# Kernel optimization log

Hardware: AMD Instinct MI355X
Metric: run time of the kernel (lower is better)

The kernel has to match this reference:

```python
import jax, jax.numpy as jnp
import numpy as np
import math

N_HEAD = 8
HIDDEN = 512
HEAD_DIM = HIDDEN // N_HEAD


def _grid_neighborhood_mask(num_nodes: int) -> jnp.ndarray:
    """Encoder mask: 2D grid adjacency (4-neighborhood) + self, with one
    extra global token (row/col 0) that attends to / is attended by all."""
    n = int(math.sqrt(num_nodes - 1))
    idx = np.arange(n * n)
    r, c = idx // n, idx % n
    # manhattan distance <= 1 <=> grid edge or self
    d = np.abs(r[:, None] - r[None, :]) + np.abs(c[:, None] - c[None, :])
    m = d <= 1  # [n*n, n*n] bool
    m = np.pad(m, ((1, 0), (1, 0)), constant_values=True)  # global token
    return jnp.asarray(m)


def setup_inputs() -> dict:
    key = jax.random.key(0)
    k_x, k_q, k_k, k_v, k_o = jax.random.split(key, 5)
    B, N = 2, 64 * 64 + 1  # 4097 nodes (64x64 grid + global token)
    scale = 1.0 / math.sqrt(HIDDEN)
    x = jax.random.normal(k_x, (B, N, HIDDEN), dtype=jnp.float32)
    Wq = jax.random.normal(k_q, (HIDDEN, HIDDEN), dtype=jnp.float32) * scale
    Wk = jax.random.normal(k_k, (HIDDEN, HIDDEN), dtype=jnp.float32) * scale
    Wv = jax.random.normal(k_v, (HIDDEN, HIDDEN), dtype=jnp.float32) * scale
    Wo = jax.random.normal(k_o, (HIDDEN, HIDDEN), dtype=jnp.float32) * scale
    return {"x": x, "Wq": Wq, "Wk": Wk, "Wv": Wv, "Wo": Wo}


def reference(x, Wq, Wk, Wv, Wo):
    B, N, D = x.shape
    mask = _grid_neighborhood_mask(N)  # [N, N] bool, static shape

    def split_heads(y):  # [B,N,D] -> [B,H,N,Dh]
        return y.reshape(B, N, N_HEAD, HEAD_DIM).transpose(0, 2, 1, 3)

    # torch Linear (no bias): y = x @ W^T
    q = split_heads(jnp.einsum('bnd,ed->bne', x, Wq))
    k = split_heads(jnp.einsum('bnd,ed->bne', x, Wk))
    v = split_heads(jnp.einsum('bnd,ed->bne', x, Wv))

    scores = jnp.einsum('bhnd,bhmd->bhnm', q, k) / math.sqrt(HEAD_DIM)
    scores = jnp.where(mask, scores, -jnp.inf)
    probs = jax.nn.softmax(scores, axis=-1)  # every row has self=True
    attn = jnp.einsum('bhnm,bhmd->bhnd', probs, v)  # [B,H,N,Dh]

    attn = attn.transpose(0, 2, 1, 3).reshape(B, N, D)
    out = jnp.einsum('bnd,ed->bne', attn, Wo)  # dropout is identity (p=0/eval)
    return out
```

## Files before the change

### kernel.cpp

```cpp
#include <hip/hip_runtime.h>

#define DI __device__ __forceinline__

typedef __bf16 bf16x8 __attribute__((ext_vector_type(8)));
typedef float  f32x4  __attribute__((ext_vector_type(4)));
typedef unsigned short u16;
typedef unsigned int   u32;

constexpr int BATCH  = 2;
constexpr int NNODE  = 4097;
constexpr int M_REAL = BATCH * NNODE;
constexpr int M_PAD  = 8448;
constexpr int KDIM   = 512;

constexpr int JC     = 256;
constexpr int NCHUNK = (NNODE + JC - 1) / JC;
constexpr int NDB    = BATCH * 8 * NCHUNK;

DI float bf2f(u16 u)  { return __uint_as_float(((u32)u) << 16); }
DI float bflo(u32 v)  { return __uint_as_float(v << 16); }
DI float bfhi(u32 v)  { return __uint_as_float(v & 0xffff0000u); }
DI u16   f2bf(float f) {
  u32 u = __float_as_uint(f);
  u32 r = (u + 0x7fffu + ((u >> 16) & 1u)) >> 16;
  return (u16)r;
}

DI void gload_lds16(const void* g, void* l) {
  __builtin_amdgcn_global_load_lds(
      (const __attribute__((address_space(1))) u32*)g,
      (__attribute__((address_space(3))) u32*)l, 16, 0, 0);
}

constexpr int NCH_X  = M_PAD * KDIM / 8;
constexpr int NCH_WQ = 1536 * KDIM / 8;
constexpr int NCH_WO = 512 * KDIM / 8;

__global__ __launch_bounds__(256) void prep(
    const float* __restrict__ x,  const float* __restrict__ wq,
    const float* __restrict__ wk, const float* __restrict__ wv,
    const float* __restrict__ wo,
    u16* __restrict__ Xp, u16* __restrict__ Wqkv, u16* __restrict__ Wob) {
  int idx = blockIdx.x * 256 + threadIdx.x;
  const float* src = nullptr;
  u16* dst = nullptr;
  bool zero = false;
  if (idx < NCH_X) {
    int row = idx >> 6;
    dst = Xp + (size_t)idx * 8;
    if (row < M_REAL) src = x + (size_t)idx * 8; else zero = true;
  } else if (idx < NCH_X + NCH_WQ) {
    int t = idx - NCH_X;
    int row = t >> 6;
    dst = Wqkv + (size_t)t * 8;
    const float* W = row < 512 ? wq : (row < 1024 ? wk : wv);
    src = W + ((size_t)(row & 511) << 9) + ((t & 63) * 8);
  } else if (idx < NCH_X + NCH_WQ + NCH_WO) {
    int t = idx - NCH_X - NCH_WQ;
    dst = Wob + (size_t)t * 8;
    src = wo + (size_t)t * 8;
  } else {
    return;
  }
  u32 o[4];
  if (zero) {
    o[0] = o[1] = o[2] = o[3] = 0u;
  } else {
    float4 f0 = ((const float4*)src)[0];
    float4 f1 = ((const float4*)src)[1];
    o[0] = (u32)f2bf(f0.x) | ((u32)f2bf(f0.y) << 16);
    o[1] = (u32)f2bf(f0.z) | ((u32)f2bf(f0.w) << 16);
    o[2] = (u32)f2bf(f1.x) | ((u32)f2bf(f1.y) << 16);
    o[3] = (u32)f2bf(f1.z) | ((u32)f2bf(f1.w) << 16);
  }
  uint4 v; v.x = o[0]; v.y = o[1]; v.z = o[2]; v.w = o[3];
  *(uint4*)dst = v;
}

__global__ __launch_bounds__(512, 2) void gemm256(
    const u16* __restrict__ A, const u16* __restrict__ B,
    u16* __restrict__ C) {
  __shared__ __align__(16) u16 SM[65536];
  const int tid  = threadIdx.x;
  const int lane = tid & 63;
  const int wid  = tid >> 6;
  const int wm   = wid >> 2;
  const int wn   = wid & 3;
  const int m0 = blockIdx.x * 256;
  const int n0 = blockIdx.y * 256;

  const int l15 = lane & 15, l7 = lane & 7, lg = lane >> 4;

  const int srow = tid >> 3;
  const int scol = ((tid & 7) ^ (srow & 7)) << 3;
  const u16* Ag = A + (size_t)(m0 + srow) * KDIM + scol;
  const u16* Bg = B + (size_t)(n0 + srow) * KDIM + scol;

  const int kx0 = ((lg * 8)        ^ (l7 << 3));
  const int kx1 = (((4 | lg) * 8)  ^ (l7 << 3));
  const int aBase = wm * 8192 + l15 * 64;
  const int bBase = 32768 + (wn >> 1) * 8192 + ((wn & 1) * 64 + l15) * 64;

  f32x4 acc[8][4] = {};

  constexpr int NT = KDIM / 64;

  auto stage = [&](int t, int buf) {
    const int ab = buf * 32768;
    const u16* ga = Ag + t * 64;
    const u16* gb = Bg + t * 64;
#pragma unroll
    for (int h = 0; h < 4; ++h) {
      gload_lds16(ga + (size_t)h * 64 * KDIM, (char*)SM + ab + h * 8192 + tid * 16);
      gload_lds16(gb + (size_t)h * 64 * KDIM, (char*)SM + 65536 + ab + h * 8192 + tid * 16);
    }
  };

  stage(0, 0);

  for (int t = 0; t < NT; ++t) {
    const int buf = t & 1;
    if (t + 1 < NT) {
      stage(t + 1, buf ^ 1);
      asm volatile("s_waitcnt vmcnt(8)" ::: "memory");
    } else {
      asm volatile("s_waitcnt vmcnt(0)" ::: "memory");
    }
    asm volatile("s_barrier" ::: "memory");

    const int aB = aBase + buf * 16384;
    const int bB = bBase + buf * 16384;

    bf16x8 bfr[4][2];
#pragma unroll
    for (int ni = 0; ni < 4; ++ni) {
      bfr[ni][0] = *(const bf16x8*)&SM[bB + ni * 1024 + kx0];
      bfr[ni][1] = *(const bf16x8*)&SM[bB + ni * 1024 + kx1];
    }
#pragma unroll
    for (int qm = 0; qm < 2; ++qm) {
      bf16x8 af[4][2];
#pragma unroll
      for (int i = 0; i < 4; ++i) {
        const int mi = qm * 4 + i;
        af[i][0] = *(const bf16x8*)&SM[aB + mi * 1024 + kx0];
        af[i][1] = *(const bf16x8*)&SM[aB + mi * 1024 + kx1];
      }
      __builtin_amdgcn_s_setprio(1);
#pragma unroll
      for (int i = 0; i < 4; ++i)
#pragma unroll
        for (int ni = 0; ni < 4; ++ni) {
          acc[qm*4+i][ni] = __builtin_amdgcn_mfma_f32_16x16x32_bf16(
              af[i][0], bfr[ni][0], acc[qm*4+i][ni], 0, 0, 0);
          acc[qm*4+i][ni] = __builtin_amdgcn_mfma_f32_16x16x32_bf16(
              af[i][1], bfr[ni][1], acc[qm*4+i][ni], 0, 0, 0);
        }
      __builtin_amdgcn_s_setprio(0);
    }
    asm volatile("s_barrier" ::: "memory");
  }

  const int cr = lg * 4, cc = l15;
#pragma unroll
  for (int mi = 0; mi < 8; ++mi)
#pragma unroll
    for (int j = 0; j < 4; ++j) {
      const int row = m0 + wm * 128 + mi * 16 + cr + j;
#pragma unroll
      for (int ni = 0; ni < 4; ++ni) {
        const int col = n0 + wn * 64 + ni * 16 + cc;
        C[(size_t)row * 1536 + col] = f2bf(acc[mi][ni][j]);
      }
    }
}

template <int N, bool OUT_F32>
__global__ __launch_bounds__(256) void gemm_bt(
    const u16* __restrict__ A, const u16* __restrict__ B,
    u16* __restrict__ Cb, float* __restrict__ Cf) {
  __shared__ __align__(16) u16 As[128 * 64];
  __shared__ __align__(16) u16 Bs[128 * 64];
  const int tid  = threadIdx.x;
  const int lane = tid & 63;
  const int wm = ((tid >> 6) >> 1) * 64;
  const int wn = ((tid >> 6) & 1) * 64;
  const int m0 = blockIdx.x * 128;
  const int n0 = blockIdx.y * 128;

  f32x4 acc[4][4] = {};

  const int rstg = tid >> 3;
  const int cstg = (tid & 7) * 8;
  const u16* Ag = A + (size_t)(m0 + rstg) * KDIM + cstg;
  const u16* Bg = B + (size_t)(n0 + rstg) * KDIM + cstg;
  char* AsB = (char*)As + tid * 16;
  char* BsB = (char*)Bs + tid * 16;

  for (int kt = 0; kt < KDIM; kt += 64) {
#pragma unroll
    for (int inst = 0; inst < 4; ++inst) {
      gload_lds16(Ag + (size_t)inst * 32 * KDIM + kt, AsB + inst * 4096);
      gload_lds16(Bg + (size_t)inst * 32 * KDIM + kt, BsB + inst * 4096);
    }
    __syncthreads();
#pragma unroll
    for (int kc = 0; kc < 2; ++kc) {
      const int ko = kc * 32 + (lane >> 4) * 8;
      bf16x8 af[4], bfr[4];
#pragma unroll
      for (int mi = 0; mi < 4; ++mi)
        af[mi] = *(const bf16x8*)&As[(wm + mi * 16 + (lane & 15)) * 64 + ko];
#pragma unroll
      for (int ni = 0; ni < 4; ++ni)
        bfr[ni] = *(const bf16x8*)&Bs[(wn + ni * 16 + (lane & 15)) * 64 + ko];
#pragma unroll
      for (int mi = 0; mi < 4; ++mi)
#pragma unroll
        for (int ni = 0; ni < 4; ++ni)
          acc[mi][ni] = __builtin_amdgcn_mfma_f32_16x16x32_bf16(
              af[mi], bfr[ni], acc[mi][ni], 0, 0, 0);
    }
    __syncthreads();
  }

  const int cr = (lane >> 4) * 4;
  const int cc = lane & 15;
#pragma unroll
  for (int mi = 0; mi < 4; ++mi) {
#pragma unroll
    for (int j = 0; j < 4; ++j) {
      const int row = m0 + wm + mi * 16 + cr + j;
      if (OUT_F32 && row >= M_REAL) continue;
#pragma unroll
      for (int ni = 0; ni < 4; ++ni) {
        const int col = n0 + wn + ni * 16 + cc;
        if constexpr (OUT_F32)
          Cf[(size_t)row * N + col] = acc[mi][ni][j];
        else
          Cb[(size_t)row * N + col] = f2bf(acc[mi][ni][j]);
      }
    }
  }
}

__global__ __launch_bounds__(256) void attn(const u16* __restrict__ QKV,
                                            u16* __restrict__ O,
                                            float* __restrict__ Part) {
  const int tid = threadIdx.x;
  if (blockIdx.x < NDB) {
    __shared__ float qs[64];
    __shared__ float ev[JC];
    __shared__ float red[256];
    const int db = blockIdx.x;
    const int b  = db / (8 * NCHUNK);
    const int rm = db % (8 * NCHUNK);
    const int h  = rm / NCHUNK;
    const int ch = rm % NCHUNK;
    const int j0 = ch * JC;
    const size_t base = (size_t)b * NNODE;

    if (tid < 64) qs[tid] = bf2f(QKV[base * 1536 + h * 64 + tid]);
    __syncthreads();

    const int j = j0 + tid;
    float s = -3e38f;
    if (j < NNODE) {
      const uint4* kp4 = (const uint4*)(QKV + (base + j) * 1536 + 512 + h * 64);
      float a = 0.f;
#pragma unroll
      for (int q8 = 0; q8 < 8; ++q8) {
        uint4 kv = kp4[q8];
        int d = q8 * 8;
        a += qs[d+0]*bflo(kv.x) + qs[d+1]*bfhi(kv.x)
           + qs[d+2]*bflo(kv.y) + qs[d+3]*bfhi(kv.y)
           + qs[d+4]*bflo(kv.z) + qs[d+5]*bfhi(kv.z)
           + qs[d+6]*bflo(kv.w) + qs[d+7]*bfhi(kv.w);
      }
      s = a * 0.125f;
    }
    red[tid] = s;
    __syncthreads();
    for (int st = 128; st > 0; st >>= 1) {
      if (tid < st) red[tid] = fmaxf(red[tid], red[tid + st]);
      __syncthreads();
    }
    const float mx = red[0];
    __syncthreads();
    const float e = (j < NNODE) ? __expf(s - mx) : 0.f;
    ev[tid] = e;
    red[tid] = e;
    __syncthreads();
    for (int st = 128; st > 0; st >>= 1) {
      if (tid < st) red[tid] += red[tid + st];
      __syncthreads();
    }
    const float ssum = red[0];
    __syncthreads();

    const int w = tid >> 6, lane = tid & 63;
    const int js = lane >> 3, dg = lane & 7;
    float oa[8] = {};
#pragma unroll
    for (int jj = 0; jj < 8; ++jj) {
      const int li = w * 64 + jj * 8 + js;
      const int jv = j0 + li;
      if (jv < NNODE) {
        const float we = ev[li];
        const uint4 vv = *(const uint4*)(QKV + (base + jv) * 1536 + 1024 + h * 64 + dg * 8);
        oa[0] += we * bflo(vv.x); oa[1] += we * bfhi(vv.x);
        oa[2] += we * bflo(vv.y); oa[3] += we * bfhi(vv.y);
        oa[4] += we * bflo(vv.z); oa[5] += we * bfhi(vv.z);
        oa[6] += we * bflo(vv.w); oa[7] += we * bfhi(vv.w);
      }
    }
#pragma unroll
    for (int m = 8; m <= 32; m <<= 1)
#pragma unroll
      for (int t = 0; t < 8; ++t) oa[t] += __shfl_xor(oa[t], m);
    __syncthreads();
    if (lane < 8) {
#pragma unroll
      for (int t = 0; t < 8; ++t) red[w * 64 + lane * 8 + t] = oa[t];
    }
    __syncthreads();
    float* P = Part + ((size_t)((b * 8 + h) * NCHUNK + ch)) * 66;
    if (tid == 0) { P[0] = mx; P[1] = ssum; }
    if (tid < 64)
      P[2 + tid] = red[tid] + red[64 + tid] + red[128 + tid] + red[192 + tid];
    return;
  }

  const int obid = blockIdx.x - NDB;
  const int sb   = ((obid & 7) << 8) | (obid >> 3);
  const int wid  = sb * 4 + (tid >> 6);
  const int lane = tid & 63;
  const int b = wid >> 12;
  const int g = wid & 4095;
  const int i = g + 1;
  const int r = g >> 6, c = g & 63;
  const size_t base = (size_t)b * NNODE;

  int  jn[6];
  bool vd[6];
  jn[0] = 0;                     vd[0] = true;
  jn[1] = i;                     vd[1] = true;
  jn[2] = (c > 0)  ? i - 1  : i; vd[2] = (c > 0);
  jn[3] = (c < 63) ? i + 1  : i; vd[3] = (c < 63);
  jn[4] = (r > 0)  ? i - 64 : i; vd[4] = (r > 0);
  jn[5] = (r < 63) ? i + 64 : i; vd[5] = (r < 63);

  const uint4 qv = *(const uint4*)(QKV + (base + i) * 1536 + lane * 8);
  float qf[8] = { bflo(qv.x), bfhi(qv.x), bflo(qv.y), bfhi(qv.y),
                  bflo(qv.z), bfhi(qv.z), bflo(qv.w), bfhi(qv.w) };

  float sc[6];
#pragma unroll
  for (int n = 0; n < 6; ++n) {
    const uint4 kv = *(const uint4*)(QKV + (base + jn[n]) * 1536 + 512 + lane * 8);
    float p = qf[0]*bflo(kv.x) + qf[1]*bfhi(kv.x)
            + qf[2]*bflo(kv.y) + qf[3]*bfhi(kv.y)
            + qf[4]*bflo(kv.z) + qf[5]*bfhi(kv.z)
            + qf[6]*bflo(kv.w) + qf[7]*bfhi(kv.w);
    p += __shfl_xor(p, 1);
    p += __shfl_xor(p, 2);
    p += __shfl_xor(p, 4);
    sc[n] = p * 0.125f;
  }
  float mx = -1e30f;
#pragma unroll
  for (int n = 0; n < 6; ++n) if (vd[n]) mx = fmaxf(mx, sc[n]);
  float pw[6], den = 0.f;
#pragma unroll
  for (int n = 0; n < 6; ++n) {
    pw[n] = vd[n] ? __expf(sc[n] - mx) : 0.f;
    den += pw[n];
  }
  const float inv = 1.f / den;

  float oa[8] = {};
#pragma unroll
  for (int n = 0; n < 6; ++n) {
    const uint4 vv = *(const uint4*)(QKV + (base + jn[n]) * 1536 + 1024 + lane * 8);
    const float w = pw[n];
    oa[0] += w * bflo(vv.x); oa[1] += w * bfhi(vv.x);
    oa[2] += w * bflo(vv.y); oa[3] += w * bfhi(vv.y);
    oa[4] += w * bflo(vv.z); oa[5] += w * bfhi(vv.z);
    oa[6] += w * bflo(vv.w); oa[7] += w * bfhi(vv.w);
  }
  uint4 ov;
  ov.x = (u32)f2bf(oa[0] * inv) | ((u32)f2bf(oa[1] * inv) << 16);
  ov.y = (u32)f2bf(oa[2] * inv) | ((u32)f2bf(oa[3] * inv) << 16);
  ov.z = (u32)f2bf(oa[4] * inv) | ((u32)f2bf(oa[5] * inv) << 16);
  ov.w = (u32)f2bf(oa[6] * inv) | ((u32)f2bf(oa[7] * inv) << 16);
  *(uint4*)(O + (base + i) * 512 + lane * 8) = ov;
}

__global__ __launch_bounds__(64) void attn_fin(const float* __restrict__ Part,
                                               u16* __restrict__ O) {
  const int b = blockIdx.x >> 3, h = blockIdx.x & 7;
  const int d = threadIdx.x;
  const float* P = Part + ((size_t)(b * 8 + h) * NCHUNK) * 66;
  float m = -3e38f;
  for (int c = 0; c < NCHUNK; ++c) m = fmaxf(m, P[c * 66]);
  float s = 0.f, o = 0.f;
  for (int c = 0; c < NCHUNK; ++c) {
    const float ex = __expf(P[c * 66] - m);
    s += P[c * 66 + 1] * ex;
    o += P[c * 66 + 2 + d] * ex;
  }
  O[(size_t)b * NNODE * 512 + h * 64 + d] = f2bf(o / s);
}

extern "C" void kernel_launch(void* const* d_in, const int* in_sizes, int n_in,
                              void* d_out, int out_size, void* d_ws, size_t ws_size,
                              hipStream_t stream) {
  (void)in_sizes; (void)n_in; (void)out_size; (void)ws_size;
  const float* x  = (const float*)d_in[0];
  const float* wq = (const float*)d_in[1];
  const float* wk = (const float*)d_in[2];
  const float* wv = (const float*)d_in[3];
  const float* wo = (const float*)d_in[4];
  float* out = (float*)d_out;

  char* ws = (char*)d_ws;
  u16* Xp   = (u16*)ws;  ws += (size_t)M_PAD * 512 * 2;
  u16* Wqkv = (u16*)ws;  ws += (size_t)1536 * 512 * 2;
  u16* Wob  = (u16*)ws;  ws += (size_t)512 * 512 * 2;
  u16* QKV  = (u16*)ws;  ws += (size_t)M_PAD * 1536 * 2;
  u16* ATT  = (u16*)ws;
  float* Part = (float*)Xp;

  prep<<<(NCH_X + NCH_WQ + NCH_WO) / 256, 256, 0, stream>>>(
      x, wq, wk, wv, wo, Xp, Wqkv, Wob);

  dim3 g1(M_PAD / 256, 1536 / 256);
  gemm256<<<g1, 512, 0, stream>>>(Xp, Wqkv, QKV);

  attn<<<NDB + 2048, 256, 0, stream>>>(QKV, ATT, Part);
  attn_fin<<<16, 64, 0, stream>>>(Part, ATT);

  dim3 g2(M_PAD / 128, 512 / 128);
  gemm_bt<512, true><<<g2, 256, 0, stream>>>(ATT, Wob, nullptr, out);
}
```

Measured before the change: 65.10 us.

## Fuse attention finalize via last-block atomic and double-buffer output GEMM

Removes the separate attn_fin launch: each global-token partial block bumps an atomic counter (zeroed in prep), and the last one merges all chunk partials. The output projection GEMM is rewritten with a double-buffered, XOR-swizzled LDS pipeline, raised priority around the MFMAs, two blocks per CU, and a grid cut to 65 row tiles, so padding rows beyond the real ones are skipped. Together these aim to save one kernel launch, hide global-to-LDS latency and reduce LDS bank conflicts. The cost is a serialized tail in the last attention block and the correctness burden of the atomic ordering and swizzle.

Measured after the change: 82.99 us. 1.27x slower.

```diff
diff --git a/kernel.cpp b/kernel.cpp
--- a/kernel.cpp
+++ b/kernel.cpp
@@ -40,8 +40,10 @@
     const float* __restrict__ x,  const float* __restrict__ wq,
     const float* __restrict__ wk, const float* __restrict__ wv,
     const float* __restrict__ wo,
-    u16* __restrict__ Xp, u16* __restrict__ Wqkv, u16* __restrict__ Wob) {
+    u16* __restrict__ Xp, u16* __restrict__ Wqkv, u16* __restrict__ Wob,
+    u32* __restrict__ Cnt) {
   int idx = blockIdx.x * 256 + threadIdx.x;
+  if (idx == 0) *Cnt = 0;
   const float* src = nullptr;
   u16* dst = nullptr;
   bool zero = false;
@@ -176,82 +178,110 @@
 }
 
 template <int N, bool OUT_F32>
-__global__ __launch_bounds__(256) void gemm_bt(
+__global__ __launch_bounds__(256, 2) void gemm128(
     const u16* __restrict__ A, const u16* __restrict__ B,
     u16* __restrict__ Cb, float* __restrict__ Cf) {
-  __shared__ __align__(16) u16 As[128 * 64];
-  __shared__ __align__(16) u16 Bs[128 * 64];
+  __shared__ __align__(16) u16 SM[32768];
   const int tid  = threadIdx.x;
   const int lane = tid & 63;
-  const int wm = ((tid >> 6) >> 1) * 64;
-  const int wn = ((tid >> 6) & 1) * 64;
-  const int m0 = blockIdx.x * 128;
-  const int n0 = blockIdx.y * 128;
+  const int wid  = tid >> 6;
+  const int wm   = wid >> 1, wn = wid & 1;
+  const int m0 = blockIdx.x * 128, n0 = blockIdx.y * 128;
+  const int l15 = lane & 15, l7 = lane & 7, lg = lane >> 4;
+
+  const int srow = tid >> 3;
+  const int scol = ((tid & 7) ^ (srow & 7)) << 3;
+  const u16* Ag = A + (size_t)(m0 + srow) * KDIM + scol;
+  const u16* Bg = B + (size_t)(n0 + srow) * KDIM + scol;
+
+  const int kx0 = ((lg * 8)       ^ (l7 << 3));
+  const int kx1 = (((4 | lg) * 8) ^ (l7 << 3));
+  const int aBase = wm * 4096 + l15 * 64;
+  const int bBase = 16384 + wn * 4096 + l15 * 64;
 
   f32x4 acc[4][4] = {};
-
-  const int rstg = tid >> 3;
-  const int cstg = (tid & 7) * 8;
-  const u16* Ag = A + (size_t)(m0 + rstg) * KDIM + cstg;
-  const u16* Bg = B + (size_t)(n0 + rstg) * KDIM + cstg;
-  char* AsB = (char*)As + tid * 16;
-  char* BsB = (char*)Bs + tid * 16;
-
-  for (int kt = 0; kt < KDIM; kt += 64) {
-#pragma unroll
-    for (int inst = 0; inst < 4; ++inst) {
-      gload_lds16(Ag + (size_t)inst * 32 * KDIM + kt, AsB + inst * 4096);
-      gload_lds16(Bg + (size_t)inst * 32 * KDIM + kt, BsB + inst * 4096);
-    }
-    __syncthreads();
-#pragma unroll
-    for (int kc = 0; kc < 2; ++kc) {
-      const int ko = kc * 32 + (lane >> 4) * 8;
-      bf16x8 af[4], bfr[4];
-#pragma unroll
-      for (int mi = 0; mi < 4; ++mi)
-        af[mi] = *(const bf16x8*)&As[(wm + mi * 16 + (lane & 15)) * 64 + ko];
-#pragma unroll
-      for (int ni = 0; ni < 4; ++ni)
-        bfr[ni] = *(const bf16x8*)&Bs[(wn + ni * 16 + (lane & 15)) * 64 + ko];
-#pragma unroll
-      for (int mi = 0; mi < 4; ++mi)
-#pragma unroll
-        for (int ni = 0; ni < 4; ++ni)
-          acc[mi][ni] = __builtin_amdgcn_mfma_f32_16x16x32_bf16(
-              af[mi], bfr[ni], acc[mi][ni], 0, 0, 0);
-    }
-    __syncthreads();
-  }
-
-  const int cr = (lane >> 4) * 4;
-  const int cc = lane & 15;
-#pragma unroll
-  for (int mi = 0; mi < 4; ++mi) {
+  constexpr int NT = KDIM / 64;
+
+  auto stage = [&](int t, int buf) {
+    const int ab = buf * 16384;
+    const u16* ga = Ag + t * 64;
+    const u16* gb = Bg + t * 64;
+#pragma unroll
+    for (int h = 0; h < 4; ++h) {
+      gload_lds16(ga + (size_t)h * 32 * KDIM, (char*)SM + ab + h * 4096 + tid * 16);
+      gload_lds16(gb + (size_t)h * 32 * KDIM, (char*)SM + 32768 + ab + h * 4096 + tid * 16);
+    }
+  };
+
+  stage(0, 0);
+
+  for (int t = 0; t < NT; ++t) {
+    const int buf = t & 1;
+    if (t + 1 < NT) {
+      stage(t + 1, buf ^ 1);
+      asm volatile("s_waitcnt vmcnt(8)" ::: "memory");
+    } else {
+      asm volatile("s_waitcnt vmcnt(0)" ::: "memory");
+    }
+    asm volatile("s_barrier" ::: "memory");
+
+    const int aB = aBase + buf * 8192;
+    const int bB = bBase + buf * 8192;
+
+    bf16x8 bfr[4][2];
+#pragma unroll
+    for (int ni = 0; ni < 4; ++ni) {
+      bfr[ni][0] = *(const bf16x8*)&SM[bB + ni * 1024 + kx0];
+      bfr[ni][1] = *(const bf16x8*)&SM[bB + ni * 1024 + kx1];
+    }
+    bf16x8 af[4][2];
+#pragma unroll
+    for (int i = 0; i < 4; ++i) {
+      af[i][0] = *(const bf16x8*)&SM[aB + i * 1024 + kx0];
+      af[i][1] = *(const bf16x8*)&SM[aB + i * 1024 + kx1];
+    }
+    __builtin_amdgcn_s_setprio(1);
+#pragma unroll
+    for (int i = 0; i < 4; ++i)
+#pragma unroll
+      for (int ni = 0; ni < 4; ++ni) {
+        acc[i][ni] = __builtin_amdgcn_mfma_f32_16x16x32_bf16(
+            af[i][0], bfr[ni][0], acc[i][ni], 0, 0, 0);
+        acc[i][ni] = __builtin_amdgcn_mfma_f32_16x16x32_bf16(
+            af[i][1], bfr[ni][1], acc[i][ni], 0, 0, 0);
+      }
+    __builtin_amdgcn_s_setprio(0);
+    asm volatile("s_barrier" ::: "memory");
+  }
+
+  const int cr = lg * 4, cc = l15;
+#pragma unroll
+  for (int mi = 0; mi < 4; ++mi)
 #pragma unroll
     for (int j = 0; j < 4; ++j) {
-      const int row = m0 + wm + mi * 16 + cr + j;
+      const int row = m0 + wm * 64 + mi * 16 + cr + j;
       if (OUT_F32 && row >= M_REAL) continue;
 #pragma unroll
       for (int ni = 0; ni < 4; ++ni) {
-        const int col = n0 + wn + ni * 16 + cc;
+        const int col = n0 + wn * 64 + ni * 16 + cc;
         if constexpr (OUT_F32)
           Cf[(size_t)row * N + col] = acc[mi][ni][j];
         else
           Cb[(size_t)row * N + col] = f2bf(acc[mi][ni][j]);
       }
     }
-  }
 }
 
 __global__ __launch_bounds__(256) void attn(const u16* __restrict__ QKV,
                                             u16* __restrict__ O,
-                                            float* __restrict__ Part) {
+                                            float* __restrict__ Part,
+                                            u32* __restrict__ Cnt) {
   const int tid = threadIdx.x;
   if (blockIdx.x < NDB) {
     __shared__ float qs[64];
     __shared__ float ev[JC];
     __shared__ float red[256];
+    __shared__ int lastFlag;
     const int db = blockIdx.x;
     const int b  = db / (8 * NCHUNK);
     const int rm = db % (8 * NCHUNK);
@@ -328,6 +358,27 @@
     if (tid == 0) { P[0] = mx; P[1] = ssum; }
     if (tid < 64)
       P[2 + tid] = red[tid] + red[64 + tid] + red[128 + tid] + red[192 + tid];
+
+    __threadfence();
+    if (tid == 0) lastFlag = (atomicAdd(Cnt, 1u) == (u32)(NDB - 1)) ? 1 : 0;
+    __syncthreads();
+    if (lastFlag) {
+      __threadfence();
+      const int d = tid & 63;
+      for (int task = tid >> 6; task < 16; task += 4) {
+        const int bb = task >> 3;
+        const float* P2 = Part + (size_t)task * NCHUNK * 66;
+        float m = -3e38f;
+        for (int c2 = 0; c2 < NCHUNK; ++c2) m = fmaxf(m, P2[c2 * 66]);
+        float ssm = 0.f, o = 0.f;
+        for (int c2 = 0; c2 < NCHUNK; ++c2) {
+          const float ex = __expf(P2[c2 * 66] - m);
+          ssm += P2[c2 * 66 + 1] * ex;
+          o   += P2[c2 * 66 + 2 + d] * ex;
+        }
+        O[(size_t)bb * NNODE * 512 + (task & 7) * 64 + d] = f2bf(o / ssm);
+      }
+    }
     return;
   }
 
@@ -396,22 +447,6 @@
   *(uint4*)(O + (base + i) * 512 + lane * 8) = ov;
 }
 
-__global__ __launch_bounds__(64) void attn_fin(const float* __restrict__ Part,
-                                               u16* __restrict__ O) {
-  const int b = blockIdx.x >> 3, h = blockIdx.x & 7;
-  const int d = threadIdx.x;
-  const float* P = Part + ((size_t)(b * 8 + h) * NCHUNK) * 66;
-  float m = -3e38f;
-  for (int c = 0; c < NCHUNK; ++c) m = fmaxf(m, P[c * 66]);
-  float s = 0.f, o = 0.f;
-  for (int c = 0; c < NCHUNK; ++c) {
-    const float ex = __expf(P[c * 66] - m);
-    s += P[c * 66 + 1] * ex;
-    o += P[c * 66 + 2 + d] * ex;
-  }
-  O[(size_t)b * NNODE * 512 + h * 64 + d] = f2bf(o / s);
-}
-
 extern "C" void kernel_launch(void* const* d_in, const int* in_sizes, int n_in,
                               void* d_out, int out_size, void* d_ws, size_t ws_size,
                               hipStream_t stream) {
@@ -430,16 +465,16 @@
   u16* QKV  = (u16*)ws;  ws += (size_t)M_PAD * 1536 * 2;
   u16* ATT  = (u16*)ws;
   float* Part = (float*)Xp;
+  u32* Cnt = (u32*)(ATT + (size_t)8320 * 512);
 
   prep<<<(NCH_X + NCH_WQ + NCH_WO) / 256, 256, 0, stream>>>(
-      x, wq, wk, wv, wo, Xp, Wqkv, Wob);
+      x, wq, wk, wv, wo, Xp, Wqkv, Wob, Cnt);
 
   dim3 g1(M_PAD / 256, 1536 / 256);
   gemm256<<<g1, 512, 0, stream>>>(Xp, Wqkv, QKV);
 
-  attn<<<NDB + 2048, 256, 0, stream>>>(QKV, ATT, Part);
-  attn_fin<<<16, 64, 0, stream>>>(Part, ATT);
-
-  dim3 g2(M_PAD / 128, 512 / 128);
-  gemm_bt<512, true><<<g2, 256, 0, stream>>>(ATT, Wob, nullptr, out);
-}
+  attn<<<NDB + 2048, 256, 0, stream>>>(QKV, ATT, Part, Cnt);
+
+  dim3 g2(65, 512 / 128);
+  gemm128<512, true><<<g2, 256, 0, stream>>>(ATT, Wob, nullptr, out);
+}
```
